# Kernel tuning notes

Measured on AMD Instinct MI355X. Metric: run time of the kernel, lower is better.

Reference implementation:

```python
import jax, jax.numpy as jnp
import numpy as np

B, T, HID, DIM, K, NQ = 8, 4096, 512, 256, 1024, 8
COMMIT_W = 1.0  # cfg commitment_weight


def setup_inputs() -> dict:
    key = jax.random.key(0)
    ks = jax.random.split(key, 4)
    rn = lambda k, shape, scale: jax.random.normal(k, shape, dtype=jnp.float32) * scale
    return {
        "x": rn(ks[0], (B, T, HID), 1.0),
        "W_in": rn(ks[1], (DIM, HID), HID ** -0.5),
        "b_in": jnp.zeros((DIM,), jnp.float32),
        "W_out": rn(ks[2], (HID, DIM), DIM ** -0.5),
        "b_out": jnp.zeros((HID,), jnp.float32),
        "codebooks": rn(ks[3], (NQ, K, DIM), 1.0),
    }


def _rvq(h, codebooks):
    """Residual VQ over NQ quantizers. h: [B,T,D]; codebooks: [NQ,K,D]."""
    def step(residual, cb):
        # squared-euclidean distance to each code: [B,T,K]
        d = (jnp.sum(residual * residual, axis=-1, keepdims=True)
             - 2.0 * jnp.einsum("btd,kd->btk", residual, cb)
             + jnp.sum(cb * cb, axis=-1))
        idx = jnp.argmin(d, axis=-1)                 # [B,T] nearest code
        q = cb[idx]                                   # [B,T,D] gather
        commit = COMMIT_W * jnp.mean((jax.lax.stop_gradient(q) - residual) ** 2)
        q_st = residual + jax.lax.stop_gradient(q - residual)  # straight-through
        return residual - q_st, (q_st, commit)

    _, (q_all, losses) = jax.lax.scan(step, h, codebooks)
    return q_all, losses  # [NQ,B,T,D], [NQ]


def reference(x, W_in, b_in, W_out, b_out, codebooks):
    h = x @ W_in.T + b_in                            # proj_in: [B,T,DIM]
    # torch code transposes to [B,D,T] for rvq and back; pure layout, math identical in [B,T,D]
    q_all, losses = _rvq(h, codebooks)
    quantized_out = q_all.sum(axis=0)                # sum of per-layer quantized
    out = quantized_out @ W_out.T + b_out            # proj_out: [B,T,HID]
    q1 = q_all[0]
    q2 = q_all[1]
    com = losses.mean()
    return out, q1, q2, com
```

## Files before the change

kernel.cpp:

```cpp
#include <hip/hip_runtime.h>

#define BT     32768
#define HIDDEN 512
#define DDIM   256
#define KCODE  1024
#define NQUANT 8

typedef _Float16 f16;
typedef _Float16 f16x8 __attribute__((ext_vector_type(8)));
typedef float f32x4 __attribute__((ext_vector_type(4)));
typedef float f32x8 __attribute__((ext_vector_type(8)));

#define LO_SCALE 64.0f
#define LO_INV   0.015625f

__global__ __launch_bounds__(256) void cb_prep2(const float* __restrict__ cb,
                                                f16* __restrict__ cbfrag,
                                                float* __restrict__ cnorm) {
  __shared__ float red[256];
  const int gc = blockIdx.x;
  const int q = gc >> 10, c = gc & 1023;
  const int chunk = c >> 6, cc = c & 63;
  const int n = cc >> 4, lj = cc & 15;
  const int d = threadIdx.x;
  const int s = d >> 5, li = (d >> 3) & 3, i = d & 7;
  const int lane = li * 16 + lj;

  const float v = cb[(size_t)gc * DDIM + d];
  const f16 hi = (f16)v;
  const f16 lo = (f16)((v - (float)hi) * LO_SCALE);
  const size_t base = ((size_t)q * 1024 + chunk * 64) * 512;
  cbfrag[base + (size_t)(s * 4 + n) * 512 + lane * 8 + i] = hi;
  cbfrag[base + (size_t)(32 + s * 4 + n) * 512 + lane * 8 + i] = lo;

  red[d] = v * v;
  __syncthreads();
  for (int t = 128; t > 0; t >>= 1) {
    if (d < t) red[d] += red[d + t];
    __syncthreads();
  }
  if (d == 0) cnorm[gc] = red[0];
}

__global__ __launch_bounds__(256) void bext_conv(const float* __restrict__ W,
                                                 f16* __restrict__ Wext,
                                                 int N, int K) {
  const int idx = blockIdx.x * 256 + threadIdx.x;
  if (idx >= N * K) return;
  const int n = idx / K, k = idx - n * K;
  const float v = W[idx];
  const f16 hi = (f16)v;
  Wext[(size_t)n * 2 * K + k] = hi;
  Wext[(size_t)n * 2 * K + K + k] = (f16)((v - (float)hi) * LO_SCALE);
}

__global__ void zero2(float* commitAcc, unsigned* bar) {
  commitAcc[0] = 0.f;
  bar[0] = 0u;
}

__global__ void finalize_com(const float* __restrict__ a, float* __restrict__ o) {
  o[0] = a[0] * (1.0f / (float)((size_t)NQUANT * BT * DDIM));
}

__device__ __forceinline__ void phase_barrier(unsigned* bar, unsigned gen,
                                              unsigned nblk) {
  __syncthreads();
  if (threadIdx.x == 0) {
    __threadfence();
    atomicAdd(bar, 1u);
    const unsigned target = gen * nblk;
    int spins = 0;
    while (__hip_atomic_load(bar, __ATOMIC_RELAXED, __HIP_MEMORY_SCOPE_AGENT) < target &&
           spins < 4096) {
      ++spins;
      __builtin_amdgcn_s_sleep(4);
    }
  }
  __syncthreads();
}

__global__ __launch_bounds__(256, 1) void rvq_fused15(
    const f16* __restrict__ rext, const f16* __restrict__ cbfrag,
    const float* __restrict__ cbf32, const float* __restrict__ cnorm,
    float* __restrict__ qsum, float* __restrict__ q1, float* __restrict__ q2,
    float* __restrict__ commitAcc, unsigned* __restrict__ bar) {
  __shared__ __align__(16) f16 Bs[2][64][512];
  __shared__ float redc[256];
  const int tid = threadIdx.x;
  const int w = tid >> 6, l = tid & 63;
  const int lj = l & 15, li = l >> 4;
  const int m0 = blockIdx.x * 128;

  f16x8 af[2][16];
#pragma unroll
  for (int m = 0; m < 2; ++m) {
    const int row = m0 + w * 32 + m * 16 + lj;
#pragma unroll
    for (int s = 0; s < 16; ++s)
      af[m][s] = *(const f16x8*)&rext[(size_t)row * 512 + s * 32 + li * 8];
  }

  float csum = 0.f;

#pragma unroll 1
  for (int nq = 0; nq < NQUANT; ++nq) {
    if (nq > 0) phase_barrier(bar, (unsigned)nq, gridDim.x);
    const f16* cbq = cbfrag + (size_t)nq * KCODE * 512;
    const float* cnq = cnorm + nq * KCODE;

    auto STAGE = [&](int chunk, int buf) {
#pragma unroll
      for (int q = 0; q < 16; ++q) {
        const int f = w * 16 + q;
        const f16* src = cbq + ((size_t)(chunk * 64 + f) << 9) + l * 8;
        __builtin_amdgcn_global_load_lds(
            (const __attribute__((address_space(1))) void*)src,
            (__attribute__((address_space(3))) void*)&Bs[buf][f][0], 16, 0, 0);
      }
    };

    float bval[2][4]; int bidxr[2][4];
#pragma unroll
    for (int m = 0; m < 2; ++m)
#pragma unroll
      for (int j = 0; j < 4; ++j) { bval[m][j] = 3.0e38f; bidxr[m][j] = 0; }

    STAGE(0, 0);
    __syncthreads();
    int buf = 0;

#pragma unroll 1
    for (int c = 0; c < 16; ++c) {
      if (c < 15) STAGE(c + 1, buf ^ 1);
      f32x4 accM[2][4], accC[2][4];
#pragma unroll
      for (int m = 0; m < 2; ++m)
#pragma unroll
        for (int n = 0; n < 4; ++n) {
          accM[m][n] = (f32x4){0.f, 0.f, 0.f, 0.f};
          accC[m][n] = (f32x4){0.f, 0.f, 0.f, 0.f};
        }

#pragma unroll
      for (int n = 0; n < 4; ++n)
#pragma unroll
        for (int s = 0; s < 8; ++s) {
          const f16x8 bf = *(const f16x8*)&Bs[buf][32 + s * 4 + n][l * 8];
#pragma unroll
          for (int m = 0; m < 2; ++m)
            accC[m][n] = __builtin_amdgcn_mfma_f32_16x16x32_f16(
                af[m][s], bf, accC[m][n], 0, 0, 0);
        }
#pragma unroll
      for (int n = 0; n < 4; ++n)
#pragma unroll
        for (int s = 0; s < 8; ++s) {
          const f16x8 bf = *(const f16x8*)&Bs[buf][s * 4 + n][l * 8];
#pragma unroll
          for (int m = 0; m < 2; ++m) {
            accC[m][n] = __builtin_amdgcn_mfma_f32_16x16x32_f16(
                af[m][8 + s], bf, accC[m][n], 0, 0, 0);
            accM[m][n] = __builtin_amdgcn_mfma_f32_16x16x32_f16(
                af[m][s], bf, accM[m][n], 0, 0, 0);
          }
        }
#pragma unroll
      for (int n = 0; n < 4; ++n) {
        const int cl = c * 64 + n * 16 + lj;
        const float cn = cnq[cl];
#pragma unroll
        for (int m = 0; m < 2; ++m)
#pragma unroll
          for (int j = 0; j < 4; ++j) {
            const float d = cn - 2.0f * (accM[m][n][j] + accC[m][n][j] * LO_INV);
            if (d < bval[m][j]) { bval[m][j] = d; bidxr[m][j] = cl; }
          }
      }
      __syncthreads();
      buf ^= 1;
    }

#pragma unroll
    for (int off = 1; off < 16; off <<= 1) {
#pragma unroll
      for (int m = 0; m < 2; ++m)
#pragma unroll
        for (int j = 0; j < 4; ++j) {
          const float ov = __shfl_xor(bval[m][j], off);
          const int oi = __shfl_xor(bidxr[m][j], off);
          if (ov < bval[m][j] || (ov == bval[m][j] && oi < bidxr[m][j])) {
            bval[m][j] = ov; bidxr[m][j] = oi;
          }
        }
    }
    const int src = (lj >> 2) * 16;
    const int sel = lj & 3;
#pragma unroll
    for (int m = 0; m < 2; ++m) {
      const int c0 = __shfl(bidxr[m][0], src);
      const int c1 = __shfl(bidxr[m][1], src);
      const int c2 = __shfl(bidxr[m][2], src);
      const int c3 = __shfl(bidxr[m][3], src);
      const int myCode = (sel == 0) ? c0 : (sel == 1) ? c1 : (sel == 2) ? c2 : c3;

      const int row = m0 + w * 32 + m * 16 + lj;
      const float* qrow = cbf32 + ((size_t)nq * KCODE + myCode) * DDIM;
#pragma unroll
      for (int s = 0; s < 8; ++s) {
        const f32x8 qv = *(const f32x8*)&qrow[s * 32 + li * 8];
        f16x8 h = af[m][s], lo = af[m][8 + s];
#pragma unroll
        for (int i = 0; i < 8; ++i) {
          const float rold = (float)h[i] + (float)lo[i] * LO_INV;
          const float diff = qv[i] - rold;
          csum += diff * diff;
          const float rnew = rold - qv[i];
          const f16 nh = (f16)rnew;
          h[i] = nh;
          lo[i] = (f16)((rnew - (float)nh) * LO_SCALE);
        }
        af[m][s] = h; af[m][8 + s] = lo;
        if (nq == 0)
          *(f32x8*)&q1[(size_t)row * DDIM + s * 32 + li * 8] = qv;
        if (nq == 1)
          *(f32x8*)&q2[(size_t)row * DDIM + s * 32 + li * 8] = qv;
      }
    }
  }

#pragma unroll
  for (int m = 0; m < 2; ++m) {
    const int row = m0 + w * 32 + m * 16 + lj;
#pragma unroll
    for (int s = 0; s < 8; ++s) {
      const f16x8 hh = *(const f16x8*)&rext[(size_t)row * 512 + s * 32 + li * 8];
      const f16x8 hl = *(const f16x8*)&rext[(size_t)row * 512 + 256 + s * 32 + li * 8];
      f32x8 o;
#pragma unroll
      for (int i = 0; i < 8; ++i)
        o[i] = ((float)hh[i] + (float)hl[i] * LO_INV) -
               ((float)af[m][s][i] + (float)af[m][8 + s][i] * LO_INV);
      *(f32x8*)&qsum[(size_t)row * DDIM + s * 32 + li * 8] = o;
    }
  }

  redc[tid] = csum;
  __syncthreads();
  for (int s = 128; s > 0; s >>= 1) {
    if (tid < s) redc[tid] += redc[tid + s];
    __syncthreads();
  }
  if (tid == 0) atomicAdd(commitAcc, redc[0]);
}

template <int K, bool WEXT>
__global__ __launch_bounds__(512) void proj3(
    const float* __restrict__ A, const f16* __restrict__ Bext,
    const float* __restrict__ bias, float* __restrict__ Cout,
    f16* __restrict__ CextOut, int Ntot) {
  __shared__ __align__(16) f16 Bs[128][512];
  const int tid = threadIdx.x;
  const int w = tid >> 6, l = tid & 63;
  const int lj = l & 15, li = l >> 4;
  const int m0 = blockIdx.x * 128;
  const int n0 = blockIdx.y * 128;
  const int row_t = m0 + w * 16 + lj;
  const int key = (lj & 7) << 4;

  f32x4 acc[8], acc2[8];
#pragma unroll
  for (int n = 0; n < 8; ++n) {
    acc[n] = (f32x4){0.f, 0.f, 0.f, 0.f};
    acc2[n] = (f32x4){0.f, 0.f, 0.f, 0.f};
  }

#pragma unroll 1
  for (int p = 0; p < K / 256; ++p) {
    __syncthreads();
#pragma unroll
    for (int q = 0; q < 16; ++q) {
      const int r = w * 16 + q;
      const int nrow = n0 + r;
      const int byteoff = (l * 16) ^ ((r & 7) << 4);
      const char* hi_base =
          (const char*)Bext + ((size_t)nrow * 2 * K + p * 256) * 2;
      const char* lo_base =
          (const char*)Bext + ((size_t)nrow * 2 * K + K + p * 256) * 2;
      const char* src = (byteoff < 512) ? hi_base + byteoff
                                        : lo_base + (byteoff - 512);
      __builtin_amdgcn_global_load_lds(
          (const __attribute__((address_space(1))) void*)src,
          (__attribute__((address_space(3))) void*)&Bs[r][0], 16, 0, 0);
    }
    f16x8 ahi[8], alo[8];
#pragma unroll
    for (int s = 0; s < 8; ++s) {
      const f32x8 v = *(const f32x8*)&A[(size_t)row_t * K + p * 256 + s * 32 + li * 8];
      f16x8 h, lo;
#pragma unroll
      for (int i = 0; i < 8; ++i) {
        const f16 hh = (f16)v[i];
        h[i] = hh;
        lo[i] = (f16)((v[i] - (float)hh) * LO_SCALE);
      }
      ahi[s] = h; alo[s] = lo;
    }
    __syncthreads();

#pragma unroll
    for (int t = 0; t < 12; ++t) {
      const int tl = (t < 4) ? t : (t < 8 ? t - 4 : t - 8);
      const int roff = (t < 4) ? 512 : 0;
#pragma unroll
      for (int n = 0; n < 8; ++n) {
        const int rr = n * 16 + lj;
#pragma unroll
        for (int kk = 0; kk < 2; ++kk) {
          const int boff = roff + tl * 128 + kk * 64 + li * 16;
          const f16x8 bf = *(const f16x8*)((const char*)&Bs[rr][0] + (boff ^ key));
          if (t < 4)
            acc2[n] = __builtin_amdgcn_mfma_f32_16x16x32_f16(ahi[2 * tl + kk], bf, acc2[n], 0, 0, 0);
          else if (t < 8)
            acc2[n] = __builtin_amdgcn_mfma_f32_16x16x32_f16(alo[2 * tl + kk], bf, acc2[n], 0, 0, 0);
          else
            acc[n] = __builtin_amdgcn_mfma_f32_16x16x32_f16(ahi[2 * tl + kk], bf, acc[n], 0, 0, 0);
        }
      }
    }
  }

#pragma unroll
  for (int n = 0; n < 8; ++n) {
    const int ncol = n0 + n * 16 + lj;
    const float bb = bias[ncol];
#pragma unroll
    for (int j = 0; j < 4; ++j) {
      const int tok = m0 + w * 16 + li * 4 + j;
      const float vv = acc[n][j] + acc2[n][j] * LO_INV + bb;
      if (WEXT) {
        const f16 hh = (f16)vv;
        CextOut[(size_t)tok * 512 + ncol] = hh;
        CextOut[(size_t)tok * 512 + 256 + ncol] = (f16)((vv - (float)hh) * LO_SCALE);
      } else {
        Cout[(size_t)tok * Ntot + ncol] = vv;
      }
    }
  }
}

extern "C" void kernel_launch(void* const* d_in, const int* in_sizes, int n_in,
                              void* d_out, int out_size, void* d_ws, size_t ws_size,
                              hipStream_t stream) {
  (void)in_sizes; (void)n_in; (void)out_size; (void)ws_size;
  const float* x     = (const float*)d_in[0];
  const float* W_in  = (const float*)d_in[1];
  const float* b_in  = (const float*)d_in[2];
  const float* W_out = (const float*)d_in[3];
  const float* b_out = (const float*)d_in[4];
  const float* cbs   = (const float*)d_in[5];

  float* out = (float*)d_out;
  float* q1  = out + (size_t)BT * HIDDEN;
  float* q2  = q1 + (size_t)BT * DDIM;
  float* com = q2 + (size_t)BT * DDIM;

  f16*   rext      = (f16*)d_ws;
  float* qsum      = (float*)(rext + (size_t)BT * 512);
  f16*   cbfrag    = (f16*)(qsum + (size_t)BT * DDIM);
  f16*   W_inext   = cbfrag + (size_t)NQUANT * KCODE * 512;
  f16*   W_outext  = W_inext + (size_t)DDIM * 1024;
  float* cnorm     = (float*)(W_outext + (size_t)HIDDEN * 512);
  float* commitAcc = cnorm + NQUANT * KCODE;
  unsigned* bar    = (unsigned*)(commitAcc + 1);

  cb_prep2<<<NQUANT * KCODE, 256, 0, stream>>>(cbs, cbfrag, cnorm);
  bext_conv<<<(DDIM * HIDDEN + 255) / 256, 256, 0, stream>>>(W_in, W_inext, DDIM, HIDDEN);
  bext_conv<<<(HIDDEN * DDIM + 255) / 256, 256, 0, stream>>>(W_out, W_outext, HIDDEN, DDIM);
  proj3<HIDDEN, true><<<dim3(BT / 128, DDIM / 128), 512, 0, stream>>>(
      x, W_inext, b_in, nullptr, rext, DDIM);
  zero2<<<1, 1, 0, stream>>>(commitAcc, bar);
  rvq_fused15<<<BT / 128, 256, 0, stream>>>(rext, cbfrag, cbs, cnorm,
                                            qsum, q1, q2, commitAcc, bar);
  proj3<DDIM, false><<<dim3(BT / 128, HIDDEN / 128), 512, 0, stream>>>(
      qsum, W_outext, b_out, out, nullptr, HIDDEN);
  finalize_com<<<1, 1, 0, stream>>>(commitAcc, com);
}
```

Baseline: 741.8 us.

## Split RVQ block work across 8 waves with one row tile per wave

```diff
diff --git a/kernel.cpp b/kernel.cpp
--- a/kernel.cpp
+++ b/kernel.cpp
@@ -80,26 +80,23 @@
   __syncthreads();
 }
 
-__global__ __launch_bounds__(256, 1) void rvq_fused15(
+__global__ __launch_bounds__(512) void rvq_fused17(
     const f16* __restrict__ rext, const f16* __restrict__ cbfrag,
     const float* __restrict__ cbf32, const float* __restrict__ cnorm,
     float* __restrict__ qsum, float* __restrict__ q1, float* __restrict__ q2,
     float* __restrict__ commitAcc, unsigned* __restrict__ bar) {
   __shared__ __align__(16) f16 Bs[2][64][512];
-  __shared__ float redc[256];
+  __shared__ float redc[512];
   const int tid = threadIdx.x;
   const int w = tid >> 6, l = tid & 63;
   const int lj = l & 15, li = l >> 4;
   const int m0 = blockIdx.x * 128;
-
-  f16x8 af[2][16];
-#pragma unroll
-  for (int m = 0; m < 2; ++m) {
-    const int row = m0 + w * 32 + m * 16 + lj;
-#pragma unroll
-    for (int s = 0; s < 16; ++s)
-      af[m][s] = *(const f16x8*)&rext[(size_t)row * 512 + s * 32 + li * 8];
-  }
+  const int row = m0 + w * 16 + lj;
+
+  f16x8 af[16];
+#pragma unroll
+  for (int s = 0; s < 16; ++s)
+    af[s] = *(const f16x8*)&rext[(size_t)row * 512 + s * 32 + li * 8];
 
   float csum = 0.f;
 
@@ -111,8 +108,8 @@
 
     auto STAGE = [&](int chunk, int buf) {
 #pragma unroll
-      for (int q = 0; q < 16; ++q) {
-        const int f = w * 16 + q;
+      for (int q = 0; q < 8; ++q) {
+        const int f = w * 8 + q;
         const f16* src = cbq + ((size_t)(chunk * 64 + f) << 9) + l * 8;
         __builtin_amdgcn_global_load_lds(
             (const __attribute__((address_space(1))) void*)src,
@@ -120,11 +117,9 @@
       }
     };
 
-    float bval[2][4]; int bidxr[2][4];
-#pragma unroll
-    for (int m = 0; m < 2; ++m)
-#pragma unroll
-      for (int j = 0; j < 4; ++j) { bval[m][j] = 3.0e38f; bidxr[m][j] = 0; }
+    float bval[4]; int bidxr[4];
+#pragma unroll
+    for (int j = 0; j < 4; ++j) { bval[j] = 3.0e38f; bidxr[j] = 0; }
 
     STAGE(0, 0);
     __syncthreads();
@@ -133,49 +128,47 @@
 #pragma unroll 1
     for (int c = 0; c < 16; ++c) {
       if (c < 15) STAGE(c + 1, buf ^ 1);
-      f32x4 accM[2][4], accC[2][4];
-#pragma unroll
-      for (int m = 0; m < 2; ++m)
-#pragma unroll
-        for (int n = 0; n < 4; ++n) {
-          accM[m][n] = (f32x4){0.f, 0.f, 0.f, 0.f};
-          accC[m][n] = (f32x4){0.f, 0.f, 0.f, 0.f};
-        }
-
-#pragma unroll
-      for (int n = 0; n < 4; ++n)
-#pragma unroll
-        for (int s = 0; s < 8; ++s) {
-          const f16x8 bf = *(const f16x8*)&Bs[buf][32 + s * 4 + n][l * 8];
-#pragma unroll
-          for (int m = 0; m < 2; ++m)
-            accC[m][n] = __builtin_amdgcn_mfma_f32_16x16x32_f16(
-                af[m][s], bf, accC[m][n], 0, 0, 0);
-        }
-#pragma unroll
-      for (int n = 0; n < 4; ++n)
-#pragma unroll
-        for (int s = 0; s < 8; ++s) {
-          const f16x8 bf = *(const f16x8*)&Bs[buf][s * 4 + n][l * 8];
-#pragma unroll
-          for (int m = 0; m < 2; ++m) {
-            accC[m][n] = __builtin_amdgcn_mfma_f32_16x16x32_f16(
-                af[m][8 + s], bf, accC[m][n], 0, 0, 0);
-            accM[m][n] = __builtin_amdgcn_mfma_f32_16x16x32_f16(
-                af[m][s], bf, accM[m][n], 0, 0, 0);
+
+#pragma unroll
+      for (int pair = 0; pair < 2; ++pair) {
+        f32x4 accM[2], accC[2];
+#pragma unroll
+        for (int np = 0; np < 2; ++np) {
+          accM[np] = (f32x4){0.f, 0.f, 0.f, 0.f};
+          accC[np] = (f32x4){0.f, 0.f, 0.f, 0.f};
+        }
+#pragma unroll
+        for (int np = 0; np < 2; ++np) {
+          const int n = pair * 2 + np;
+#pragma unroll
+          for (int s = 0; s < 8; ++s) {
+            const f16x8 bf = *(const f16x8*)&Bs[buf][32 + s * 4 + n][l * 8];
+            accC[np] = __builtin_amdgcn_mfma_f32_16x16x32_f16(
+                af[s], bf, accC[np], 0, 0, 0);
           }
         }
 #pragma unroll
-      for (int n = 0; n < 4; ++n) {
-        const int cl = c * 64 + n * 16 + lj;
-        const float cn = cnq[cl];
-#pragma unroll
-        for (int m = 0; m < 2; ++m)
+        for (int np = 0; np < 2; ++np) {
+          const int n = pair * 2 + np;
+#pragma unroll
+          for (int s = 0; s < 8; ++s) {
+            const f16x8 bf = *(const f16x8*)&Bs[buf][s * 4 + n][l * 8];
+            accC[np] = __builtin_amdgcn_mfma_f32_16x16x32_f16(
+                af[8 + s], bf, accC[np], 0, 0, 0);
+            accM[np] = __builtin_amdgcn_mfma_f32_16x16x32_f16(
+                af[s], bf, accM[np], 0, 0, 0);
+          }
+        }
+#pragma unroll
+        for (int np = 0; np < 2; ++np) {
+          const int cl = c * 64 + (pair * 2 + np) * 16 + lj;
+          const float cn = cnq[cl];
 #pragma unroll
           for (int j = 0; j < 4; ++j) {
-            const float d = cn - 2.0f * (accM[m][n][j] + accC[m][n][j] * LO_INV);
-            if (d < bval[m][j]) { bval[m][j] = d; bidxr[m][j] = cl; }
+            const float d = cn - 2.0f * (accM[np][j] + accC[np][j] * LO_INV);
+            if (d < bval[j]) { bval[j] = d; bidxr[j] = cl; }
           }
+        }
       }
       __syncthreads();
       buf ^= 1;
@@ -184,70 +177,60 @@
 #pragma unroll
     for (int off = 1; off < 16; off <<= 1) {
 #pragma unroll
-      for (int m = 0; m < 2; ++m)
-#pragma unroll
-        for (int j = 0; j < 4; ++j) {
-          const float ov = __shfl_xor(bval[m][j], off);
-          const int oi = __shfl_xor(bidxr[m][j], off);
-          if (ov < bval[m][j] || (ov == bval[m][j] && oi < bidxr[m][j])) {
-            bval[m][j] = ov; bidxr[m][j] = oi;
-          }
-        }
+      for (int j = 0; j < 4; ++j) {
+        const float ov = __shfl_xor(bval[j], off);
+        const int oi = __shfl_xor(bidxr[j], off);
+        if (ov < bval[j] || (ov == bval[j] && oi < bidxr[j])) {
+          bval[j] = ov; bidxr[j] = oi;
+        }
+      }
     }
     const int src = (lj >> 2) * 16;
+    const int c0 = __shfl(bidxr[0], src);
+    const int c1 = __shfl(bidxr[1], src);
+    const int c2 = __shfl(bidxr[2], src);
+    const int c3 = __shfl(bidxr[3], src);
     const int sel = lj & 3;
-#pragma unroll
-    for (int m = 0; m < 2; ++m) {
-      const int c0 = __shfl(bidxr[m][0], src);
-      const int c1 = __shfl(bidxr[m][1], src);
-      const int c2 = __shfl(bidxr[m][2], src);
-      const int c3 = __shfl(bidxr[m][3], src);
-      const int myCode = (sel == 0) ? c0 : (sel == 1) ? c1 : (sel == 2) ? c2 : c3;
-
-      const int row = m0 + w * 32 + m * 16 + lj;
-      const float* qrow = cbf32 + ((size_t)nq * KCODE + myCode) * DDIM;
-#pragma unroll
-      for (int s = 0; s < 8; ++s) {
-        const f32x8 qv = *(const f32x8*)&qrow[s * 32 + li * 8];
-        f16x8 h = af[m][s], lo = af[m][8 + s];
-#pragma unroll
-        for (int i = 0; i < 8; ++i) {
-          const float rold = (float)h[i] + (float)lo[i] * LO_INV;
-          const float diff = qv[i] - rold;
-          csum += diff * diff;
-          const float rnew = rold - qv[i];
-          const f16 nh = (f16)rnew;
-          h[i] = nh;
-          lo[i] = (f16)((rnew - (float)nh) * LO_SCALE);
-        }
-        af[m][s] = h; af[m][8 + s] = lo;
-        if (nq == 0)
-          *(f32x8*)&q1[(size_t)row * DDIM + s * 32 + li * 8] = qv;
-        if (nq == 1)
-          *(f32x8*)&q2[(size_t)row * DDIM + s * 32 + li * 8] = qv;
-      }
-    }
-  }
-
-#pragma unroll
-  for (int m = 0; m < 2; ++m) {
-    const int row = m0 + w * 32 + m * 16 + lj;
+    const int myCode = (sel == 0) ? c0 : (sel == 1) ? c1 : (sel == 2) ? c2 : c3;
+
+    const float* qrow = cbf32 + ((size_t)nq * KCODE + myCode) * DDIM;
 #pragma unroll
     for (int s = 0; s < 8; ++s) {
-      const f16x8 hh = *(const f16x8*)&rext[(size_t)row * 512 + s * 32 + li * 8];
-      const f16x8 hl = *(const f16x8*)&rext[(size_t)row * 512 + 256 + s * 32 + li * 8];
-      f32x8 o;
-#pragma unroll
-      for (int i = 0; i < 8; ++i)
-        o[i] = ((float)hh[i] + (float)hl[i] * LO_INV) -
-               ((float)af[m][s][i] + (float)af[m][8 + s][i] * LO_INV);
-      *(f32x8*)&qsum[(size_t)row * DDIM + s * 32 + li * 8] = o;
-    }
+      const f32x8 qv = *(const f32x8*)&qrow[s * 32 + li * 8];
+      f16x8 h = af[s], lo = af[8 + s];
+#pragma unroll
+      for (int i = 0; i < 8; ++i) {
+        const float rold = (float)h[i] + (float)lo[i] * LO_INV;
+        const float diff = qv[i] - rold;
+        csum += diff * diff;
+        const float rnew = rold - qv[i];
+        const f16 nh = (f16)rnew;
+        h[i] = nh;
+        lo[i] = (f16)((rnew - (float)nh) * LO_SCALE);
+      }
+      af[s] = h; af[8 + s] = lo;
+      if (nq == 0)
+        *(f32x8*)&q1[(size_t)row * DDIM + s * 32 + li * 8] = qv;
+      if (nq == 1)
+        *(f32x8*)&q2[(size_t)row * DDIM + s * 32 + li * 8] = qv;
+    }
+  }
+
+#pragma unroll
+  for (int s = 0; s < 8; ++s) {
+    const f16x8 hh = *(const f16x8*)&rext[(size_t)row * 512 + s * 32 + li * 8];
+    const f16x8 hl = *(const f16x8*)&rext[(size_t)row * 512 + 256 + s * 32 + li * 8];
+    f32x8 o;
+#pragma unroll
+    for (int i = 0; i < 8; ++i)
+      o[i] = ((float)hh[i] + (float)hl[i] * LO_INV) -
+             ((float)af[s][i] + (float)af[8 + s][i] * LO_INV);
+    *(f32x8*)&qsum[(size_t)row * DDIM + s * 32 + li * 8] = o;
   }
 
   redc[tid] = csum;
   __syncthreads();
-  for (int s = 128; s > 0; s >>= 1) {
+  for (int s = 256; s > 0; s >>= 1) {
     if (tid < s) redc[tid] += redc[tid + s];
     __syncthreads();
   }
@@ -380,7 +363,7 @@
   proj3<HIDDEN, true><<<dim3(BT / 128, DDIM / 128), 512, 0, stream>>>(
       x, W_inext, b_in, nullptr, rext, DDIM);
   zero2<<<1, 1, 0, stream>>>(commitAcc, bar);
-  rvq_fused15<<<BT / 128, 256, 0, stream>>>(rext, cbfrag, cbs, cnorm,
+  rvq_fused17<<<BT / 128, 512, 0, stream>>>(rext, cbfrag, cbs, cnorm,
                                             qsum, q1, q2, commitAcc, bar);
   proj3<DDIM, false><<<dim3(BT / 128, HIDDEN / 128), 512, 0, stream>>>(
       qsum, W_outext, b_out, out, nullptr, HIDDEN);
```

Measured after the change: 704.4 us (median of 2 runs). -5.0%, faster.
